# Performance work log

Hardware: AMD Instinct MI355X
Metric: run time of the kernel (lower is better)

## Reference

```python
import jax, jax.numpy as jnp
import numpy as np

CH = 512
GROUPS = 32
EPS = 1e-6


def setup_inputs() -> dict:
    key = jax.random.key(0)
    ks = jax.random.split(key, 12)
    b, c, h, w = 4, CH, 64, 64
    std = 1.0 / np.sqrt(c)
    return {
        "x": jax.random.normal(ks[0], (b, c, h, w), dtype=jnp.float32),
        "norm_gamma": jnp.ones((c,), jnp.float32),
        "norm_beta": jnp.zeros((c,), jnp.float32),
        "wq": jax.random.normal(ks[1], (c, c), jnp.float32) * std,
        "bq": jax.random.normal(ks[2], (c,), jnp.float32) * 0.01,
        "wk": jax.random.normal(ks[3], (c, c), jnp.float32) * std,
        "bk": jax.random.normal(ks[4], (c,), jnp.float32) * 0.01,
        "wv": jax.random.normal(ks[5], (c, c), jnp.float32) * std,
        "bv": jax.random.normal(ks[6], (c,), jnp.float32) * 0.01,
        "wo": jax.random.normal(ks[7], (c, c), jnp.float32) * std,
        "bo": jax.random.normal(ks[8], (c,), jnp.float32) * 0.01,
    }


def _group_norm(x, gamma, beta):
    b, c, h, w = x.shape
    xg = x.reshape(b, GROUPS, c // GROUPS, h, w)
    mean = xg.mean(axis=(2, 3, 4), keepdims=True)
    var = xg.var(axis=(2, 3, 4), keepdims=True)
    xn = ((xg - mean) * jax.lax.rsqrt(var + EPS)).reshape(b, c, h, w)
    return xn * gamma[None, :, None, None] + beta[None, :, None, None]


def reference(x, norm_gamma, norm_beta, wq, bq, wk, bk, wv, bv, wo, bo):
    b, c, h, w = x.shape
    hn = _group_norm(x, norm_gamma, norm_beta)
    hs = hn.reshape(b, c, h * w)  # [b, c, n]
    # 1x1 convs == per-pixel matmuls over channel dim (weight[out,in])
    q = jnp.einsum('oc,bcn->bno', wq, hs) + bq  # [b, n, c]
    k = jnp.einsum('oc,bcn->bon', wk, hs) + bk[None, :, None]  # [b, c, n]
    v = jnp.einsum('oc,bcn->bno', wv, hs) + bv  # [b, n, c]
    scale = c ** (-0.5)
    attn = jax.nn.softmax(jnp.einsum('bnc,bcm->bnm', q, k) * scale, axis=-1)
    out = jnp.einsum('bnm,bmc->bnc', attn, v)  # [b, n, c]
    out = jnp.einsum('oc,bnc->bon', wo, out) + bo[None, :, None]  # [b, c, n]
    return x + out.reshape(b, c, h, w)
```

## Files before the change

### kernel.cpp

```cpp
#include <hip/hip_runtime.h>
#include <hip/hip_bf16.h>
#include <cstdint>

typedef __bf16 bf16;
typedef __bf16 bf16x8 __attribute__((ext_vector_type(8)));
typedef __bf16 bf16x4 __attribute__((ext_vector_type(4)));
typedef float f32x4 __attribute__((ext_vector_type(4)));

__device__ __forceinline__ void gld_lds16(const void* g, void* l) {
  __builtin_amdgcn_global_load_lds((const __attribute__((address_space(1))) void*)g,
                                   (__attribute__((address_space(3))) void*)l, 16, 0, 0);
}

enum { BIAS_NONE = 0, BIAS_COL = 1, BIAS_ROW = 2, BIAS_QK = 3 };
enum { OUT_BF16 = 0, OUT_F32_RESID = 1, OUT_EXP = 2 };

template<int BIAS_MODE, int OUT_MODE>
__global__ __launch_bounds__(256)
void gemm_bt(const bf16* __restrict__ A, long sA, int lda,
             const bf16* __restrict__ Bm, long sB, int ldb,
             void* __restrict__ Cv, long sC, int ldc,
             const float* __restrict__ bias, const float* __restrict__ bias2,
             const float* __restrict__ resid, long sR,
             int K, float scale)
{
  const int bm = blockIdx.x, bn = blockIdx.y, bz = blockIdx.z;
  const char* Ab = (const char*)(A + (long)bz * sA);
  const char* Bb = (const char*)(Bm + (long)bz * sB);
  const int tid = threadIdx.x;
  const int wave = tid >> 6, lane = tid & 63;
  const int wr = wave >> 1, wc = wave & 1;

  __shared__ __attribute__((aligned(128))) char lds[32768];
  char* ldsA = lds;
  char* ldsB = lds + 16384;

  uint32_t aoff[4], boff[4];
#pragma unroll
  for (int i = 0; i < 4; ++i) {
    uint32_t ra = (uint32_t)(wr * 64 + i * 16 + (lane & 15));
    uint32_t la = ra * 128u + (uint32_t)((lane >> 4) << 4);
    aoff[i] = la ^ ((la >> 3) & 0x70u);
    uint32_t rb = (uint32_t)(wc * 64 + i * 16 + (lane & 15));
    uint32_t lb = rb * 128u + (uint32_t)((lane >> 4) << 4);
    boff[i] = lb ^ ((lb >> 3) & 0x70u);
  }
  uint32_t srow[4], sinb[4];
#pragma unroll
  for (int t = 0; t < 4; ++t) {
    uint32_t paddr = (uint32_t)(((wave * 4 + t) * 64 + lane) * 16);
    uint32_t laddr = paddr ^ ((paddr >> 3) & 0x70u);
    srow[t] = laddr >> 7;
    sinb[t] = laddr & 127u;
  }

  const long ldab = (long)lda * 2, ldbb = (long)ldb * 2;
  const long arow0 = (long)bm * 128, brow0 = (long)bn * 128;
  f32x4 acc[4][4] = {};
  const int nK = K >> 6;
  for (int kt = 0; kt < nK; ++kt) {
    const long k0b = (long)kt * 128;
#pragma unroll
    for (int t = 0; t < 4; ++t) {
      gld_lds16(Ab + (arow0 + srow[t]) * ldab + k0b + sinb[t], ldsA + (wave * 4 + t) * 1024);
      gld_lds16(Bb + (brow0 + srow[t]) * ldbb + k0b + sinb[t], ldsB + (wave * 4 + t) * 1024);
    }
    __syncthreads();
#pragma unroll
    for (int kk = 0; kk < 2; ++kk) {
      bf16x8 af[4], bfr[4];
#pragma unroll
      for (int i = 0; i < 4; ++i) {
        af[i]  = *(const bf16x8*)(ldsA + (aoff[i] ^ (kk << 6)));
        bfr[i] = *(const bf16x8*)(ldsB + (boff[i] ^ (kk << 6)));
      }
#pragma unroll
      for (int mi = 0; mi < 4; ++mi)
#pragma unroll
        for (int ni = 0; ni < 4; ++ni)
          acc[mi][ni] = __builtin_amdgcn_mfma_f32_16x16x32_bf16(af[mi], bfr[ni], acc[mi][ni], 0, 0, 0);
    }
    __syncthreads();
  }

  const int cl = lane & 15, rq = lane >> 4;
  const long row0 = (long)bm * 128 + wr * 64;
  const long col0 = (long)bn * 128 + wc * 64;

  if constexpr (OUT_MODE == OUT_F32_RESID) {
    float* Co = (float*)Cv + (long)bz * sC;
    const float* X = resid + (long)bz * sR;
#pragma unroll
    for (int mi = 0; mi < 4; ++mi)
#pragma unroll
      for (int ni = 0; ni < 4; ++ni) {
        const long col = col0 + ni * 16 + cl;
#pragma unroll
        for (int j = 0; j < 4; ++j) {
          const long row = row0 + mi * 16 + rq * 4 + j;
          Co[row * ldc + col] = acc[mi][ni][j] + bias[row] + X[row * ldc + col];
        }
      }
  } else if constexpr (BIAS_MODE == BIAS_QK) {
    const bool isq = (col0 < 512);
    bf16* base = (bf16*)Cv + (long)bz * sC + (isq ? 0 : sR);
    const long csub = isq ? 0 : 512;
#pragma unroll
    for (int mi = 0; mi < 4; ++mi)
#pragma unroll
      for (int ni = 0; ni < 4; ++ni) {
        const long col = col0 + ni * 16 + cl;
        const float bc = isq ? bias[col] * scale : bias2[col - 512];
        const float vs = isq ? scale : 1.f;
#pragma unroll
        for (int j = 0; j < 4; ++j) {
          const long row = row0 + mi * 16 + rq * 4 + j;
          base[row * ldc + (col - csub)] = (bf16)(acc[mi][ni][j] * vs + bc);
        }
      }
  } else {
    bf16* Co = (bf16*)Cv + (long)bz * sC;
#pragma unroll
    for (int mi = 0; mi < 4; ++mi)
#pragma unroll
      for (int ni = 0; ni < 4; ++ni) {
        const long col = col0 + ni * 16 + cl;
        float bc = 0.f;
        if (BIAS_MODE == BIAS_COL) bc = bias[col] * scale;
#pragma unroll
        for (int j = 0; j < 4; ++j) {
          const long row = row0 + mi * 16 + rq * 4 + j;
          float v = acc[mi][ni][j] * (BIAS_MODE == BIAS_COL ? scale : 1.f) + bc;
          if (BIAS_MODE == BIAS_ROW) v += bias[row];
          if constexpr (OUT_MODE == OUT_EXP) v = __expf(v);
          Co[row * ldc + col] = (bf16)v;
        }
      }
  }
}

__global__ __launch_bounds__(256, 2)
void gemm_pv7(const bf16* __restrict__ P, long sA,
              const bf16* __restrict__ Vm, long sB,
              bf16* __restrict__ O, long sC, int swz)
{
  constexpr int T = 64;
  extern __shared__ char lds[];
  char* ldsA = lds;
  char* ldsB = lds + 16384;

  int bm, bn, bz;
  if (swz) {
    const int bid = blockIdx.x;
    const int xcd = bid & 7;
    bz = xcd >> 1;
    bn = (bid >> 3) & 1;
    bm = ((bid >> 4) << 1) | (xcd & 1);
  } else { bm = blockIdx.x; bn = blockIdx.y; bz = blockIdx.z; }

  const char* Ab = (const char*)(P + (long)bz * sA) + (long)bm * 64 * 8192;
  const char* Bb = (const char*)(Vm + (long)bz * sB) + (long)bn * 256 * 8192;
  const int tid = threadIdx.x, wave = tid >> 6, lane = tid & 63;
  const int lg = lane >> 4, l15 = lane & 15;

  const uint32_t ar0 = (uint32_t)(tid >> 3), ac16 = (uint32_t)((tid & 7) * 16);
  const uint32_t aswz = (ar0 & 7) << 4;

  const uint32_t bdst0 = (uint32_t)tid * 16;

  uint32_t aO[4], bO[4];
#pragma unroll
  for (int mi = 0; mi < 4; ++mi) {
    uint32_t r = (uint32_t)(mi * 16 + l15);
    aO[mi] = r * 128 + (((uint32_t)(lg * 16)) ^ ((r & 7) << 4));
  }
#pragma unroll
  for (int ni = 0; ni < 4; ++ni) {
    uint32_t r = (uint32_t)(wave * 64 + ni * 16 + l15);
    bO[ni] = r * 128 + (((uint32_t)(lg * 16)) ^ ((r & 7) << 4));
  }

  f32x4 acc[4][4] = {};
  float lsum0 = 0.f, lsum1 = 0.f;

  auto stageB = [&](uint32_t nb, int t) {
#pragma unroll
    for (int j = 0; j < 8; ++j) {
      uint32_t row = (uint32_t)(j * 32) + ar0;
      gld_lds16(Bb + (long)row * 8192 + (long)t * 128 + (ac16 ^ ((row & 7) << 4)),
                ldsB + nb * 32768 + (uint32_t)(j * 4096) + bdst0);
    }
  };
  auto loadA0 = [&](int t) -> bf16x8 {
    return *(const bf16x8*)(Ab + (long)ar0 * 8192 + (long)t * 128 + ac16);
  };
  auto loadA1 = [&](int t) -> bf16x8 {
    return *(const bf16x8*)(Ab + (long)(32 + ar0) * 8192 + (long)t * 128 + ac16);
  };
  auto writeA = [&](uint32_t nb, bf16x8 p0, bf16x8 p1) {
#pragma unroll
    for (int j = 0; j < 8; ++j) {
      lsum0 += (float)p0[j];
      lsum1 += (float)p1[j];
    }
    *(bf16x8*)(ldsA + nb * 8192 + ar0 * 128 + (ac16 ^ aswz)) = p0;
    *(bf16x8*)(ldsA + nb * 8192 + (32 + ar0) * 128 + (ac16 ^ aswz)) = p1;
  };

  bf16x8 an0 = loadA0(0), an1 = loadA1(0);
  stageB(0, 0);
  writeA(0, an0, an1);
  an0 = loadA0(1); an1 = loadA1(1);
  asm volatile("s_waitcnt vmcnt(2)" ::: "memory");
  asm volatile("s_waitcnt lgkmcnt(0)" ::: "memory");
  __builtin_amdgcn_sched_barrier(0);
  __builtin_amdgcn_s_barrier();

  for (int t = 0; t < T; ++t) {
    const uint32_t cur = (uint32_t)(t & 1), nxt = cur ^ 1u;

    if (t + 1 < T) stageB(nxt, t + 1);
    if (t + 1 < T) writeA(nxt, an0, an1);
    if (t + 2 < T) { an0 = loadA0(t + 2); an1 = loadA1(t + 2); }

    bf16x8 af[4][2], bfr[4][2];
#pragma unroll
    for (int mi = 0; mi < 4; ++mi)
#pragma unroll
      for (int kk = 0; kk < 2; ++kk)
        af[mi][kk] = *(const bf16x8*)(ldsA + ((cur * 8192 + aO[mi]) ^ (uint32_t)(kk << 6)));
#pragma unroll
    for (int ni = 0; ni < 4; ++ni)
#pragma unroll
      for (int kk = 0; kk < 2; ++kk)
        bfr[ni][kk] = *(const bf16x8*)(ldsB + ((cur * 32768 + bO[ni]) ^ (uint32_t)(kk << 6)));

    __builtin_amdgcn_s_setprio(1);
#pragma unroll
    for (int mi = 0; mi < 4; ++mi)
#pragma unroll
      for (int ni = 0; ni < 4; ++ni)
#pragma unroll
        for (int kk = 0; kk < 2; ++kk)
          acc[mi][ni] = __builtin_amdgcn_mfma_f32_16x16x32_bf16(af[mi][kk], bfr[ni][kk], acc[mi][ni], 0, 0, 0);
    __builtin_amdgcn_s_setprio(0);

    if (t + 1 < T) {
      if (t + 2 < T) asm volatile("s_waitcnt vmcnt(2)" ::: "memory");
      else           asm volatile("s_waitcnt vmcnt(0)" ::: "memory");
      asm volatile("s_waitcnt lgkmcnt(0)" ::: "memory");
      __builtin_amdgcn_sched_barrier(0);
      __builtin_amdgcn_s_barrier();
    }
  }

  lsum0 += __shfl_xor(lsum0, 1, 64);
  lsum0 += __shfl_xor(lsum0, 2, 64);
  lsum0 += __shfl_xor(lsum0, 4, 64);
  lsum1 += __shfl_xor(lsum1, 1, 64);
  lsum1 += __shfl_xor(lsum1, 2, 64);
  lsum1 += __shfl_xor(lsum1, 4, 64);
  float* Lrow = (float*)ldsA;
  if ((tid & 7) == 0) {
    Lrow[ar0] = lsum0;
    Lrow[32 + ar0] = lsum1;
  }
  __syncthreads();

  bf16* Co = O + (long)bz * sC + (long)bm * 64 * 512 + (long)bn * 256;
#pragma unroll
  for (int mi = 0; mi < 4; ++mi)
#pragma unroll
    for (int j = 0; j < 4; ++j) {
      const int row = mi * 16 + lg * 4 + j;
      const float invL = 1.f / Lrow[row];
#pragma unroll
      for (int ni = 0; ni < 4; ++ni) {
        const int col = wave * 64 + ni * 16 + l15;
        Co[(long)row * 512 + col] = (bf16)(acc[mi][ni][j] * invL);
      }
    }
}

__global__ __launch_bounds__(256)
void gn_stats(const float* __restrict__ x, float* __restrict__ stats)
{
  const int bg = blockIdx.x;
  const float4* px = (const float4*)(x + (long)bg * 65536);
  float s1 = 0.f, s2 = 0.f;
  for (int i = threadIdx.x; i < 16384; i += 256) {
    float4 f = px[i];
    s1 += f.x + f.y + f.z + f.w;
    s2 += f.x * f.x + f.y * f.y + f.z * f.z + f.w * f.w;
  }
#pragma unroll
  for (int d = 32; d > 0; d >>= 1) {
    s1 += __shfl_xor(s1, d, 64);
    s2 += __shfl_xor(s2, d, 64);
  }
  __shared__ float r1[4], r2[4];
  const int wave = threadIdx.x >> 6, lane = threadIdx.x & 63;
  if (lane == 0) { r1[wave] = s1; r2[wave] = s2; }
  __syncthreads();
  if (threadIdx.x == 0) {
    float t1 = r1[0] + r1[1] + r1[2] + r1[3];
    float t2 = r2[0] + r2[1] + r2[2] + r2[3];
    float mean = t1 * (1.f / 65536.f);
    float var  = t2 * (1.f / 65536.f) - mean * mean;
    stats[bg * 2]     = mean;
    stats[bg * 2 + 1] = rsqrtf(var + 1e-6f);
  }
}

__global__ __launch_bounds__(256)
void gn_apply(const float* __restrict__ x, const float* __restrict__ stats,
              const float* __restrict__ gamma, const float* __restrict__ beta,
              bf16* __restrict__ hn)
{
  const int b = blockIdx.y;
  const int n0 = blockIdx.x * 64;
  __shared__ __attribute__((aligned(16))) char lt[65536];
  const int tid = threadIdx.x;
  for (int i = 0; i < 32; ++i) {
    int f = i * 256 + tid;
    int c = f >> 4;
    int n4 = f & 15;
    float4 xv = *(const float4*)(x + (((long)b * 512 + c) * 4096) + n0 + n4 * 4);
    int g = c >> 4;
    float mean = stats[(b * 32 + g) * 2];
    float rstd = stats[(b * 32 + g) * 2 + 1];
    float ga = gamma[c], be = beta[c];
    float y[4];
    y[0] = (xv.x - mean) * rstd * ga + be;
    y[1] = (xv.y - mean) * rstd * ga + be;
    y[2] = (xv.z - mean) * rstd * ga + be;
    y[3] = (xv.w - mean) * rstd * ga + be;
    uint32_t cb = (uint32_t)(c * 2);
#pragma unroll
    for (int jj = 0; jj < 4; ++jj) {
      uint32_t nl = (uint32_t)(n4 * 4 + jj);
      uint32_t phys = nl * 1024u + (cb ^ (((nl >> 2) & 7u) << 4));
      *(bf16*)(lt + phys) = (bf16)y[jj];
    }
  }
  __syncthreads();
  for (int i = 0; i < 16; ++i) {
    int j = i * 256 + tid;
    uint32_t row = (uint32_t)(j >> 6);
    uint32_t m = (uint32_t)(j & 63);
    uint32_t phys = row * 1024u + ((m * 16u) ^ (((row >> 2) & 7u) << 4));
    uint4 val = *(const uint4*)(lt + phys);
    *(uint4*)((char*)(hn + ((long)b * 4096 + n0 + row) * 512) + m * 16) = val;
  }
}

__global__ __launch_bounds__(256)
void conv_w4(const float* __restrict__ w0, const float* __restrict__ w1,
             const float* __restrict__ w2, const float* __restrict__ w3,
             bf16* __restrict__ dst)
{
  const int z = blockIdx.y;
  const float* src = (z == 0) ? w0 : (z == 1) ? w1 : (z == 2) ? w2 : w3;
  const int i = blockIdx.x * 256 + threadIdx.x;
  float4 f = ((const float4*)src)[i];
  bf16x4 o;
  o[0] = (bf16)f.x; o[1] = (bf16)f.y; o[2] = (bf16)f.z; o[3] = (bf16)f.w;
  ((bf16x4*)(dst))[(long)z * 65536 + i] = o;
}

extern "C" void kernel_launch(void* const* d_in, const int* in_sizes, int n_in,
                              void* d_out, int out_size, void* d_ws, size_t ws_size,
                              hipStream_t stream)
{
  const float* x     = (const float*)d_in[0];
  const float* gamma = (const float*)d_in[1];
  const float* beta  = (const float*)d_in[2];
  const float* wq = (const float*)d_in[3];
  const float* bq = (const float*)d_in[4];
  const float* wk = (const float*)d_in[5];
  const float* bk = (const float*)d_in[6];
  const float* wv = (const float*)d_in[7];
  const float* bv = (const float*)d_in[8];
  const float* wo = (const float*)d_in[9];
  const float* bo = (const float*)d_in[10];
  float* out = (float*)d_out;

  char* ws = (char*)d_ws;
  bf16* hn  = (bf16*)(ws + 0);
  bf16* q   = (bf16*)(ws + 16777216);
  bf16* k   = (bf16*)(ws + 33554432);
  bf16* v   = (bf16*)(ws + 50331648);
  bf16* O   = (bf16*)(ws + 67108864);
  bf16* wqb = (bf16*)(ws + 83886080);
  bf16* wvb = (bf16*)(ws + 84934656);
  bf16* wob = (bf16*)(ws + 85458944);
  float* gstats = (float*)(ws + 85983232);
  bf16* S   = (bf16*)(ws + 85984256);

  const long sBC = 2097152;
  const long sS1 = 16777216;
  const long K_OFS = 8388608;
  const float scale = 0.044194173824159216f;

  const int LDS_PV = 81920;
  hipFuncSetAttribute(reinterpret_cast<const void*>(gemm_pv7),
                      hipFuncAttributeMaxDynamicSharedMemorySize, LDS_PV);

  conv_w4<<<dim3(256, 4), 256, 0, stream>>>(wq, wk, wv, wo, wqb);
  gn_stats<<<128, 256, 0, stream>>>(x, gstats);
  gn_apply<<<dim3(64, 4), 256, 0, stream>>>(x, gstats, gamma, beta, hn);

  gemm_bt<BIAS_QK, OUT_BF16><<<dim3(32, 8, 4), 256, 0, stream>>>(
      hn, sBC, 512, wqb, 0, 512, q, sBC, 512,
      bq, bk, nullptr, K_OFS, 512, scale);
  gemm_bt<BIAS_ROW, OUT_BF16><<<dim3(4, 32, 4), 256, 0, stream>>>(
      wvb, 0, 512, hn, sBC, 512, v, sBC, 4096,
      bv, nullptr, nullptr, 0, 512, 1.f);

  const bool tier1 = ws_size >= (size_t)220202112;
  if (tier1) {
    gemm_bt<BIAS_NONE, OUT_EXP><<<dim3(32, 32, 4), 256, 0, stream>>>(
        q, sBC, 512, k, sBC, 512, S, sS1, 4096,
        nullptr, nullptr, nullptr, 0, 512, 1.f);
    gemm_pv7<<<dim3(512, 1, 1), 256, LDS_PV, stream>>>(
        S, sS1, v, sBC, O, sBC, 1);
  } else {
    for (int b = 0; b < 4; ++b) {
      gemm_bt<BIAS_NONE, OUT_EXP><<<dim3(32, 32, 1), 256, 0, stream>>>(
          q + b * sBC, 0, 512, k + b * sBC, 0, 512, S, 0, 4096,
          nullptr, nullptr, nullptr, 0, 512, 1.f);
      gemm_pv7<<<dim3(64, 2, 1), 256, LDS_PV, stream>>>(
          S, 0, v + b * sBC, 0, O + b * sBC, 0, 0);
    }
  }

  gemm_bt<BIAS_ROW, OUT_F32_RESID><<<dim3(4, 32, 4), 256, 0, stream>>>(
      wob, 0, 512, O, sBC, 512, out, sBC, 4096,
      bo, nullptr, x, sBC, 512, 1.f);
}
```

Measured before the change: 269.2 us.

## Halve PV K-tile to raise occupancy and swizzle QK^T blocks across XCDs

The PV kernel now uses a 32-wide K step (128 iterations instead of 64), with a new LDS layout, a new swizzle and half the LDS footprint. This allows launch bounds of 4 blocks per CU instead of 2, to improve latency hiding. The QK^T exp GEMM now runs on a flattened 1D grid that is remapped so neighbouring M-tiles land on the same XCD, to improve L2 reuse of the K operand. The trade-off is twice as many barriers per PV tile and lower register headroom per thread.

```diff
diff --git a/kernel.cpp b/kernel.cpp
--- a/kernel.cpp
+++ b/kernel.cpp
@@ -22,9 +22,17 @@
              void* __restrict__ Cv, long sC, int ldc,
              const float* __restrict__ bias, const float* __restrict__ bias2,
              const float* __restrict__ resid, long sR,
-             int K, float scale)
-{
-  const int bm = blockIdx.x, bn = blockIdx.y, bz = blockIdx.z;
+             int K, float scale, int swz)
+{
+  int bm, bn, bz;
+  if (swz) {
+    const int bid = blockIdx.x;
+    const int xcd = bid & 7;
+    const int i = bid >> 3;
+    bm = xcd * 4 + (i & 3);
+    bn = (i >> 2) & 31;
+    bz = i >> 7;
+  } else { bm = blockIdx.x; bn = blockIdx.y; bz = blockIdx.z; }
   const char* Ab = (const char*)(A + (long)bz * sA);
   const char* Bb = (const char*)(Bm + (long)bz * sB);
   const int tid = threadIdx.x;
@@ -37,13 +45,13 @@
 
   uint32_t aoff[4], boff[4];
 #pragma unroll
-  for (int i = 0; i < 4; ++i) {
-    uint32_t ra = (uint32_t)(wr * 64 + i * 16 + (lane & 15));
+  for (int i2 = 0; i2 < 4; ++i2) {
+    uint32_t ra = (uint32_t)(wr * 64 + i2 * 16 + (lane & 15));
     uint32_t la = ra * 128u + (uint32_t)((lane >> 4) << 4);
-    aoff[i] = la ^ ((la >> 3) & 0x70u);
-    uint32_t rb = (uint32_t)(wc * 64 + i * 16 + (lane & 15));
+    aoff[i2] = la ^ ((la >> 3) & 0x70u);
+    uint32_t rb = (uint32_t)(wc * 64 + i2 * 16 + (lane & 15));
     uint32_t lb = rb * 128u + (uint32_t)((lane >> 4) << 4);
-    boff[i] = lb ^ ((lb >> 3) & 0x70u);
+    boff[i2] = lb ^ ((lb >> 3) & 0x70u);
   }
   uint32_t srow[4], sinb[4];
 #pragma unroll
@@ -70,9 +78,9 @@
     for (int kk = 0; kk < 2; ++kk) {
       bf16x8 af[4], bfr[4];
 #pragma unroll
-      for (int i = 0; i < 4; ++i) {
-        af[i]  = *(const bf16x8*)(ldsA + (aoff[i] ^ (kk << 6)));
-        bfr[i] = *(const bf16x8*)(ldsB + (boff[i] ^ (kk << 6)));
+      for (int i2 = 0; i2 < 4; ++i2) {
+        af[i2]  = *(const bf16x8*)(ldsA + (aoff[i2] ^ (kk << 6)));
+        bfr[i2] = *(const bf16x8*)(ldsB + (boff[i2] ^ (kk << 6)));
       }
 #pragma unroll
       for (int mi = 0; mi < 4; ++mi)
@@ -139,15 +147,15 @@
   }
 }
 
-__global__ __launch_bounds__(256, 2)
-void gemm_pv7(const bf16* __restrict__ P, long sA,
+__global__ __launch_bounds__(256, 4)
+void gemm_pv8(const bf16* __restrict__ P, long sA,
               const bf16* __restrict__ Vm, long sB,
               bf16* __restrict__ O, long sC, int swz)
 {
-  constexpr int T = 64;
+  constexpr int T = 128;
   extern __shared__ char lds[];
   char* ldsA = lds;
-  char* ldsB = lds + 16384;
+  char* ldsB = lds + 8192;
 
   int bm, bn, bz;
   if (swz) {
@@ -163,55 +171,46 @@
   const int tid = threadIdx.x, wave = tid >> 6, lane = tid & 63;
   const int lg = lane >> 4, l15 = lane & 15;
 
-  const uint32_t ar0 = (uint32_t)(tid >> 3), ac16 = (uint32_t)((tid & 7) * 16);
-  const uint32_t aswz = (ar0 & 7) << 4;
-
-  const uint32_t bdst0 = (uint32_t)tid * 16;
+  const uint32_t ar = (uint32_t)(tid >> 2), ach = (uint32_t)((tid & 3) * 16);
+  const uint32_t aswz = ((ar >> 1) & 3u) << 4;
 
   uint32_t aO[4], bO[4];
 #pragma unroll
   for (int mi = 0; mi < 4; ++mi) {
     uint32_t r = (uint32_t)(mi * 16 + l15);
-    aO[mi] = r * 128 + (((uint32_t)(lg * 16)) ^ ((r & 7) << 4));
+    aO[mi] = r * 64 + (((uint32_t)(lg * 16)) ^ (((r >> 1) & 3u) << 4));
   }
 #pragma unroll
   for (int ni = 0; ni < 4; ++ni) {
     uint32_t r = (uint32_t)(wave * 64 + ni * 16 + l15);
-    bO[ni] = r * 128 + (((uint32_t)(lg * 16)) ^ ((r & 7) << 4));
+    bO[ni] = r * 64 + (((uint32_t)(lg * 16)) ^ (((r >> 1) & 3u) << 4));
   }
 
   f32x4 acc[4][4] = {};
-  float lsum0 = 0.f, lsum1 = 0.f;
+  float lsum = 0.f;
 
   auto stageB = [&](uint32_t nb, int t) {
 #pragma unroll
-    for (int j = 0; j < 8; ++j) {
-      uint32_t row = (uint32_t)(j * 32) + ar0;
-      gld_lds16(Bb + (long)row * 8192 + (long)t * 128 + (ac16 ^ ((row & 7) << 4)),
-                ldsB + nb * 32768 + (uint32_t)(j * 4096) + bdst0);
+    for (int j = 0; j < 4; ++j) {
+      uint32_t row = (uint32_t)(j * 64) + ar;
+      gld_lds16(Bb + (long)row * 8192 + (long)t * 64 + (ach ^ (((row >> 1) & 3u) << 4)),
+                ldsB + nb * 16384 + (uint32_t)(j * 4096) + (uint32_t)tid * 16);
     }
   };
-  auto loadA0 = [&](int t) -> bf16x8 {
-    return *(const bf16x8*)(Ab + (long)ar0 * 8192 + (long)t * 128 + ac16);
+  auto loadA = [&](int t) -> bf16x8 {
+    return *(const bf16x8*)(Ab + (long)ar * 8192 + (long)t * 64 + ach);
   };
-  auto loadA1 = [&](int t) -> bf16x8 {
-    return *(const bf16x8*)(Ab + (long)(32 + ar0) * 8192 + (long)t * 128 + ac16);
+  auto writeA = [&](uint32_t nb, bf16x8 p) {
+#pragma unroll
+    for (int j = 0; j < 8; ++j) lsum += (float)p[j];
+    *(bf16x8*)(ldsA + nb * 4096 + ar * 64 + (ach ^ aswz)) = p;
   };
-  auto writeA = [&](uint32_t nb, bf16x8 p0, bf16x8 p1) {
-#pragma unroll
-    for (int j = 0; j < 8; ++j) {
-      lsum0 += (float)p0[j];
-      lsum1 += (float)p1[j];
-    }
-    *(bf16x8*)(ldsA + nb * 8192 + ar0 * 128 + (ac16 ^ aswz)) = p0;
-    *(bf16x8*)(ldsA + nb * 8192 + (32 + ar0) * 128 + (ac16 ^ aswz)) = p1;
-  };
-
-  bf16x8 an0 = loadA0(0), an1 = loadA1(0);
+
+  bf16x8 an = loadA(0);
   stageB(0, 0);
-  writeA(0, an0, an1);
-  an0 = loadA0(1); an1 = loadA1(1);
-  asm volatile("s_waitcnt vmcnt(2)" ::: "memory");
+  writeA(0, an);
+  an = loadA(1);
+  asm volatile("s_waitcnt vmcnt(1)" ::: "memory");
   asm volatile("s_waitcnt lgkmcnt(0)" ::: "memory");
   __builtin_amdgcn_sched_barrier(0);
   __builtin_amdgcn_s_barrier();
@@ -220,33 +219,27 @@
     const uint32_t cur = (uint32_t)(t & 1), nxt = cur ^ 1u;
 
     if (t + 1 < T) stageB(nxt, t + 1);
-    if (t + 1 < T) writeA(nxt, an0, an1);
-    if (t + 2 < T) { an0 = loadA0(t + 2); an1 = loadA1(t + 2); }
-
-    bf16x8 af[4][2], bfr[4][2];
+    if (t + 1 < T) writeA(nxt, an);
+    if (t + 2 < T) an = loadA(t + 2);
+
+    bf16x8 af[4], bfr[4];
 #pragma unroll
     for (int mi = 0; mi < 4; ++mi)
-#pragma unroll
-      for (int kk = 0; kk < 2; ++kk)
-        af[mi][kk] = *(const bf16x8*)(ldsA + ((cur * 8192 + aO[mi]) ^ (uint32_t)(kk << 6)));
+      af[mi] = *(const bf16x8*)(ldsA + cur * 4096 + aO[mi]);
 #pragma unroll
     for (int ni = 0; ni < 4; ++ni)
-#pragma unroll
-      for (int kk = 0; kk < 2; ++kk)
-        bfr[ni][kk] = *(const bf16x8*)(ldsB + ((cur * 32768 + bO[ni]) ^ (uint32_t)(kk << 6)));
+      bfr[ni] = *(const bf16x8*)(ldsB + cur * 16384 + bO[ni]);
 
     __builtin_amdgcn_s_setprio(1);
 #pragma unroll
     for (int mi = 0; mi < 4; ++mi)
 #pragma unroll
       for (int ni = 0; ni < 4; ++ni)
-#pragma unroll
-        for (int kk = 0; kk < 2; ++kk)
-          acc[mi][ni] = __builtin_amdgcn_mfma_f32_16x16x32_bf16(af[mi][kk], bfr[ni][kk], acc[mi][ni], 0, 0, 0);
+        acc[mi][ni] = __builtin_amdgcn_mfma_f32_16x16x32_bf16(af[mi], bfr[ni], acc[mi][ni], 0, 0, 0);
     __builtin_amdgcn_s_setprio(0);
 
     if (t + 1 < T) {
-      if (t + 2 < T) asm volatile("s_waitcnt vmcnt(2)" ::: "memory");
+      if (t + 2 < T) asm volatile("s_waitcnt vmcnt(1)" ::: "memory");
       else           asm volatile("s_waitcnt vmcnt(0)" ::: "memory");
       asm volatile("s_waitcnt lgkmcnt(0)" ::: "memory");
       __builtin_amdgcn_sched_barrier(0);
@@ -254,17 +247,10 @@
     }
   }
 
-  lsum0 += __shfl_xor(lsum0, 1, 64);
-  lsum0 += __shfl_xor(lsum0, 2, 64);
-  lsum0 += __shfl_xor(lsum0, 4, 64);
-  lsum1 += __shfl_xor(lsum1, 1, 64);
-  lsum1 += __shfl_xor(lsum1, 2, 64);
-  lsum1 += __shfl_xor(lsum1, 4, 64);
+  lsum += __shfl_xor(lsum, 1, 64);
+  lsum += __shfl_xor(lsum, 2, 64);
   float* Lrow = (float*)ldsA;
-  if ((tid & 7) == 0) {
-    Lrow[ar0] = lsum0;
-    Lrow[32 + ar0] = lsum1;
-  }
+  if ((tid & 3) == 0) Lrow[ar] = lsum;
   __syncthreads();
 
   bf16* Co = O + (long)bz * sC + (long)bm * 64 * 512 + (long)bn * 256;
@@ -402,8 +388,8 @@
   const long K_OFS = 8388608;
   const float scale = 0.044194173824159216f;
 
-  const int LDS_PV = 81920;
-  hipFuncSetAttribute(reinterpret_cast<const void*>(gemm_pv7),
+  const int LDS_PV = 40960;
+  hipFuncSetAttribute(reinterpret_cast<const void*>(gemm_pv8),
                       hipFuncAttributeMaxDynamicSharedMemorySize, LDS_PV);
 
   conv_w4<<<dim3(256, 4), 256, 0, stream>>>(wq, wk, wv, wo, wqb);
@@ -412,29 +398,29 @@
 
   gemm_bt<BIAS_QK, OUT_BF16><<<dim3(32, 8, 4), 256, 0, stream>>>(
       hn, sBC, 512, wqb, 0, 512, q, sBC, 512,
-      bq, bk, nullptr, K_OFS, 512, scale);
+      bq, bk, nullptr, K_OFS, 512, scale, 0);
   gemm_bt<BIAS_ROW, OUT_BF16><<<dim3(4, 32, 4), 256, 0, stream>>>(
       wvb, 0, 512, hn, sBC, 512, v, sBC, 4096,
-      bv, nullptr, nullptr, 0, 512, 1.f);
+      bv, nullptr, nullptr, 0, 512, 1.f, 0);
 
   const bool tier1 = ws_size >= (size_t)220202112;
   if (tier1) {
-    gemm_bt<BIAS_NONE, OUT_EXP><<<dim3(32, 32, 4), 256, 0, stream>>>(
+    gemm_bt<BIAS_NONE, OUT_EXP><<<dim3(4096, 1, 1), 256, 0, stream>>>(
         q, sBC, 512, k, sBC, 512, S, sS1, 4096,
-        nullptr, nullptr, nullptr, 0, 512, 1.f);
-    gemm_pv7<<<dim3(512, 1, 1), 256, LDS_PV, stream>>>(
+        nullptr, nullptr, nullptr, 0, 512, 1.f, 1);
+    gemm_pv8<<<dim3(512, 1, 1), 256, LDS_PV, stream>>>(
         S, sS1, v, sBC, O, sBC, 1);
   } else {
     for (int b = 0; b < 4; ++b) {
       gemm_bt<BIAS_NONE, OUT_EXP><<<dim3(32, 32, 1), 256, 0, stream>>>(
           q + b * sBC, 0, 512, k + b * sBC, 0, 512, S, 0, 4096,
-          nullptr, nullptr, nullptr, 0, 512, 1.f);
-      gemm_pv7<<<dim3(64, 2, 1), 256, LDS_PV, stream>>>(
+          nullptr, nullptr, nullptr, 0, 512, 1.f, 0);
+      gemm_pv8<<<dim3(64, 2, 1), 256, LDS_PV, stream>>>(
           S, 0, v + b * sBC, 0, O + b * sBC, 0, 0);
     }
   }
 
   gemm_bt<BIAS_ROW, OUT_F32_RESID><<<dim3(4, 32, 4), 256, 0, stream>>>(
       wob, 0, 512, O, sBC, 512, out, sBC, 4096,
-      bo, nullptr, x, sBC, 512, 1.f);
-}
+      bo, nullptr, x, sBC, 512, 1.f, 0);
+}
```

Result: slower. 299.4 us (+11.2%).

## Load P fragments directly into registers and compute row sums via MFMA with ones

Applied to the files above, without the earlier changes.

The PV GEMM kernel stops staging the P (exp-scores) tile through LDS. Each wave now loads its A fragments straight from global memory into double-buffered registers. The softmax row sums are computed with an extra MFMA against a ones vector instead of scalar adds, shuffles and an LDS reduction. This cuts LDS traffic and usage (64KB instead of 80KB) and removes the final sync, at the cost of every wave redundantly loading the same P rows from global or cache and using more registers.

```diff
diff --git a/kernel.cpp b/kernel.cpp
--- a/kernel.cpp
+++ b/kernel.cpp
@@ -140,14 +140,13 @@
 }
 
 __global__ __launch_bounds__(256, 2)
-void gemm_pv7(const bf16* __restrict__ P, long sA,
-              const bf16* __restrict__ Vm, long sB,
-              bf16* __restrict__ O, long sC, int swz)
+void gemm_pv10(const bf16* __restrict__ P, long sA,
+               const bf16* __restrict__ Vm, long sB,
+               bf16* __restrict__ O, long sC, int swz)
 {
   constexpr int T = 64;
   extern __shared__ char lds[];
-  char* ldsA = lds;
-  char* ldsB = lds + 16384;
+  char* ldsB = lds;
 
   int bm, bn, bz;
   if (swz) {
@@ -164,16 +163,14 @@
   const int lg = lane >> 4, l15 = lane & 15;
 
   const uint32_t ar0 = (uint32_t)(tid >> 3), ac16 = (uint32_t)((tid & 7) * 16);
-  const uint32_t aswz = (ar0 & 7) << 4;
-
   const uint32_t bdst0 = (uint32_t)tid * 16;
 
-  uint32_t aO[4], bO[4];
-#pragma unroll
-  for (int mi = 0; mi < 4; ++mi) {
-    uint32_t r = (uint32_t)(mi * 16 + l15);
-    aO[mi] = r * 128 + (((uint32_t)(lg * 16)) ^ ((r & 7) << 4));
-  }
+  const char* aBase[4];
+#pragma unroll
+  for (int mi = 0; mi < 4; ++mi)
+    aBase[mi] = Ab + (long)(mi * 16 + l15) * 8192 + lg * 16;
+
+  uint32_t bO[4];
 #pragma unroll
   for (int ni = 0; ni < 4; ++ni) {
     uint32_t r = (uint32_t)(wave * 64 + ni * 16 + l15);
@@ -181,7 +178,10 @@
   }
 
   f32x4 acc[4][4] = {};
-  float lsum0 = 0.f, lsum1 = 0.f;
+  f32x4 acc_l[4] = {};
+  bf16x8 ones;
+#pragma unroll
+  for (int j = 0; j < 8; ++j) ones[j] = (bf16)1.0f;
 
   auto stageB = [&](uint32_t nb, int t) {
 #pragma unroll
@@ -191,44 +191,27 @@
                 ldsB + nb * 32768 + (uint32_t)(j * 4096) + bdst0);
     }
   };
-  auto loadA0 = [&](int t) -> bf16x8 {
-    return *(const bf16x8*)(Ab + (long)ar0 * 8192 + (long)t * 128 + ac16);
+  auto loadA = [&](bf16x8 (&a)[4][2], int t) {
+#pragma unroll
+    for (int mi = 0; mi < 4; ++mi)
+#pragma unroll
+      for (int kk = 0; kk < 2; ++kk)
+        a[mi][kk] = *(const bf16x8*)(aBase[mi] + (long)t * 128 + kk * 64);
   };
-  auto loadA1 = [&](int t) -> bf16x8 {
-    return *(const bf16x8*)(Ab + (long)(32 + ar0) * 8192 + (long)t * 128 + ac16);
-  };
-  auto writeA = [&](uint32_t nb, bf16x8 p0, bf16x8 p1) {
-#pragma unroll
-    for (int j = 0; j < 8; ++j) {
-      lsum0 += (float)p0[j];
-      lsum1 += (float)p1[j];
-    }
-    *(bf16x8*)(ldsA + nb * 8192 + ar0 * 128 + (ac16 ^ aswz)) = p0;
-    *(bf16x8*)(ldsA + nb * 8192 + (32 + ar0) * 128 + (ac16 ^ aswz)) = p1;
-  };
-
-  bf16x8 an0 = loadA0(0), an1 = loadA1(0);
+
+  bf16x8 aE[4][2], aO_[4][2];
+
   stageB(0, 0);
-  writeA(0, an0, an1);
-  an0 = loadA0(1); an1 = loadA1(1);
-  asm volatile("s_waitcnt vmcnt(2)" ::: "memory");
-  asm volatile("s_waitcnt lgkmcnt(0)" ::: "memory");
+  loadA(aE, 0);
+  asm volatile("s_waitcnt vmcnt(8)" ::: "memory");
   __builtin_amdgcn_sched_barrier(0);
   __builtin_amdgcn_s_barrier();
 
-  for (int t = 0; t < T; ++t) {
+  auto body = [&](int t, bf16x8 (&aUse)[4][2], bf16x8 (&aNxt)[4][2]) {
     const uint32_t cur = (uint32_t)(t & 1), nxt = cur ^ 1u;
-
-    if (t + 1 < T) stageB(nxt, t + 1);
-    if (t + 1 < T) writeA(nxt, an0, an1);
-    if (t + 2 < T) { an0 = loadA0(t + 2); an1 = loadA1(t + 2); }
-
-    bf16x8 af[4][2], bfr[4][2];
-#pragma unroll
-    for (int mi = 0; mi < 4; ++mi)
-#pragma unroll
-      for (int kk = 0; kk < 2; ++kk)
-        af[mi][kk] = *(const bf16x8*)(ldsA + ((cur * 8192 + aO[mi]) ^ (uint32_t)(kk << 6)));
+    if (t + 1 < T) { stageB(nxt, t + 1); loadA(aNxt, t + 1); }
+
+    bf16x8 bfr[4][2];
 #pragma unroll
     for (int ni = 0; ni < 4; ++ni)
 #pragma unroll
@@ -237,35 +220,29 @@
 
     __builtin_amdgcn_s_setprio(1);
 #pragma unroll
-    for (int mi = 0; mi < 4; ++mi)
-#pragma unroll
-      for (int ni = 0; ni < 4; ++ni)
-#pragma unroll
-        for (int kk = 0; kk < 2; ++kk)
-          acc[mi][ni] = __builtin_amdgcn_mfma_f32_16x16x32_bf16(af[mi][kk], bfr[ni][kk], acc[mi][ni], 0, 0, 0);
+    for (int kk = 0; kk < 2; ++kk)
+#pragma unroll
+      for (int mi = 0; mi < 4; ++mi) {
+        acc_l[mi] = __builtin_amdgcn_mfma_f32_16x16x32_bf16(aUse[mi][kk], ones, acc_l[mi], 0, 0, 0);
+#pragma unroll
+        for (int ni = 0; ni < 4; ++ni)
+          acc[mi][ni] = __builtin_amdgcn_mfma_f32_16x16x32_bf16(aUse[mi][kk], bfr[ni][kk], acc[mi][ni], 0, 0, 0);
+      }
     __builtin_amdgcn_s_setprio(0);
 
     if (t + 1 < T) {
-      if (t + 2 < T) asm volatile("s_waitcnt vmcnt(2)" ::: "memory");
-      else           asm volatile("s_waitcnt vmcnt(0)" ::: "memory");
+      asm volatile("s_waitcnt vmcnt(8)" ::: "memory");
       asm volatile("s_waitcnt lgkmcnt(0)" ::: "memory");
       __builtin_amdgcn_sched_barrier(0);
       __builtin_amdgcn_s_barrier();
     }
-  }
-
-  lsum0 += __shfl_xor(lsum0, 1, 64);
-  lsum0 += __shfl_xor(lsum0, 2, 64);
-  lsum0 += __shfl_xor(lsum0, 4, 64);
-  lsum1 += __shfl_xor(lsum1, 1, 64);
-  lsum1 += __shfl_xor(lsum1, 2, 64);
-  lsum1 += __shfl_xor(lsum1, 4, 64);
-  float* Lrow = (float*)ldsA;
-  if ((tid & 7) == 0) {
-    Lrow[ar0] = lsum0;
-    Lrow[32 + ar0] = lsum1;
-  }
-  __syncthreads();
+  };
+
+#pragma unroll 1
+  for (int t2 = 0; t2 < T; t2 += 2) {
+    body(t2, aE, aO_);
+    body(t2 + 1, aO_, aE);
+  }
 
   bf16* Co = O + (long)bz * sC + (long)bm * 64 * 512 + (long)bn * 256;
 #pragma unroll
@@ -273,7 +250,7 @@
 #pragma unroll
     for (int j = 0; j < 4; ++j) {
       const int row = mi * 16 + lg * 4 + j;
-      const float invL = 1.f / Lrow[row];
+      const float invL = 1.f / acc_l[mi][j];
 #pragma unroll
       for (int ni = 0; ni < 4; ++ni) {
         const int col = wave * 64 + ni * 16 + l15;
@@ -402,8 +379,8 @@
   const long K_OFS = 8388608;
   const float scale = 0.044194173824159216f;
 
-  const int LDS_PV = 81920;
-  hipFuncSetAttribute(reinterpret_cast<const void*>(gemm_pv7),
+  const int LDS_PV = 65536;
+  hipFuncSetAttribute(reinterpret_cast<const void*>(gemm_pv10),
                       hipFuncAttributeMaxDynamicSharedMemorySize, LDS_PV);
 
   conv_w4<<<dim3(256, 4), 256, 0, stream>>>(wq, wk, wv, wo, wqb);
@@ -422,14 +399,14 @@
     gemm_bt<BIAS_NONE, OUT_EXP><<<dim3(32, 32, 4), 256, 0, stream>>>(
         q, sBC, 512, k, sBC, 512, S, sS1, 4096,
         nullptr, nullptr, nullptr, 0, 512, 1.f);
-    gemm_pv7<<<dim3(512, 1, 1), 256, LDS_PV, stream>>>(
+    gemm_pv10<<<dim3(512, 1, 1), 256, LDS_PV, stream>>>(
         S, sS1, v, sBC, O, sBC, 1);
   } else {
     for (int b = 0; b < 4; ++b) {
       gemm_bt<BIAS_NONE, OUT_EXP><<<dim3(32, 32, 1), 256, 0, stream>>>(
           q + b * sBC, 0, 512, k + b * sBC, 0, 512, S, 0, 4096,
           nullptr, nullptr, nullptr, 0, 512, 1.f);
-      gemm_pv7<<<dim3(64, 2, 1), 256, LDS_PV, stream>>>(
+      gemm_pv10<<<dim3(64, 2, 1), 256, LDS_PV, stream>>>(
           S, 0, v + b * sBC, 0, O + b * sBC, 0, 0);
     }
   }
```

Measured after the change: 343.6 us. +27.6%, slower.

## Store V pre-tiled and load PV B-operand directly from global into registers

Applied to the files above, without the earlier changes.

The V projection now writes V in a k-blocked tiled layout (8 contiguous channels per 16-byte chunk), so the PV kernel can fetch B fragments straight from global memory into registers instead of staging them through LDS. This cuts LDS from 80KB to 16KB per block, removing the B LDS writes and reads and the associated waits, with registers double-buffered across an unrolled pair of iterations. The cost is that each wave reads B directly from global/L2 with no intra-block sharing, and the V epilogue now does scattered stores.

```diff
diff --git a/kernel.cpp b/kernel.cpp
--- a/kernel.cpp
+++ b/kernel.cpp
@@ -13,7 +13,7 @@
 }
 
 enum { BIAS_NONE = 0, BIAS_COL = 1, BIAS_ROW = 2, BIAS_QK = 3 };
-enum { OUT_BF16 = 0, OUT_F32_RESID = 1, OUT_EXP = 2 };
+enum { OUT_BF16 = 0, OUT_F32_RESID = 1, OUT_EXP = 2, OUT_VTILED = 3 };
 
 template<int BIAS_MODE, int OUT_MODE>
 __global__ __launch_bounds__(256)
@@ -101,6 +101,20 @@
           Co[row * ldc + col] = acc[mi][ni][j] + bias[row] + X[row * ldc + col];
         }
       }
+  } else if constexpr (OUT_MODE == OUT_VTILED) {
+    bf16* Vt = (bf16*)Cv + (long)bz * sC;
+#pragma unroll
+    for (int mi = 0; mi < 4; ++mi)
+#pragma unroll
+      for (int ni = 0; ni < 4; ++ni) {
+        const long col = col0 + ni * 16 + cl;
+#pragma unroll
+        for (int j = 0; j < 4; ++j) {
+          const long row = row0 + mi * 16 + rq * 4 + j;
+          float v = acc[mi][ni][j] + bias[row];
+          Vt[((col >> 3) * 512 + row) * 8 + (col & 7)] = (bf16)v;
+        }
+      }
   } else if constexpr (BIAS_MODE == BIAS_QK) {
     const bool isq = (col0 < 512);
     bf16* base = (bf16*)Cv + (long)bz * sC + (isq ? 0 : sR);
@@ -140,14 +154,13 @@
 }
 
 __global__ __launch_bounds__(256, 2)
-void gemm_pv7(const bf16* __restrict__ P, long sA,
-              const bf16* __restrict__ Vm, long sB,
-              bf16* __restrict__ O, long sC, int swz)
+void gemm_pv11(const bf16* __restrict__ P, long sA,
+               const bf16* __restrict__ Vt, long sVt,
+               bf16* __restrict__ O, long sC, int swz)
 {
   constexpr int T = 64;
   extern __shared__ char lds[];
   char* ldsA = lds;
-  char* ldsB = lds + 16384;
 
   int bm, bn, bz;
   if (swz) {
@@ -159,37 +172,35 @@
   } else { bm = blockIdx.x; bn = blockIdx.y; bz = blockIdx.z; }
 
   const char* Ab = (const char*)(P + (long)bz * sA) + (long)bm * 64 * 8192;
-  const char* Bb = (const char*)(Vm + (long)bz * sB) + (long)bn * 256 * 8192;
+  const char* Btb = (const char*)(Vt + (long)bz * sVt);
   const int tid = threadIdx.x, wave = tid >> 6, lane = tid & 63;
   const int lg = lane >> 4, l15 = lane & 15;
 
   const uint32_t ar0 = (uint32_t)(tid >> 3), ac16 = (uint32_t)((tid & 7) * 16);
   const uint32_t aswz = (ar0 & 7) << 4;
 
-  const uint32_t bdst0 = (uint32_t)tid * 16;
-
-  uint32_t aO[4], bO[4];
+  uint32_t aO[4];
 #pragma unroll
   for (int mi = 0; mi < 4; ++mi) {
     uint32_t r = (uint32_t)(mi * 16 + l15);
     aO[mi] = r * 128 + (((uint32_t)(lg * 16)) ^ ((r & 7) << 4));
   }
+  uint32_t colb[4];
 #pragma unroll
   for (int ni = 0; ni < 4; ++ni) {
-    uint32_t r = (uint32_t)(wave * 64 + ni * 16 + l15);
-    bO[ni] = r * 128 + (((uint32_t)(lg * 16)) ^ ((r & 7) << 4));
+    uint32_t col = (uint32_t)(bn * 256 + wave * 64 + ni * 16 + l15);
+    colb[ni] = col * 16 + (uint32_t)lg * 8192;
   }
 
   f32x4 acc[4][4] = {};
   float lsum0 = 0.f, lsum1 = 0.f;
 
-  auto stageB = [&](uint32_t nb, int t) {
-#pragma unroll
-    for (int j = 0; j < 8; ++j) {
-      uint32_t row = (uint32_t)(j * 32) + ar0;
-      gld_lds16(Bb + (long)row * 8192 + (long)t * 128 + (ac16 ^ ((row & 7) << 4)),
-                ldsB + nb * 32768 + (uint32_t)(j * 4096) + bdst0);
-    }
+  auto loadB = [&](bf16x8 (&b)[4][2], int t) {
+#pragma unroll
+    for (int ni = 0; ni < 4; ++ni)
+#pragma unroll
+      for (int kk = 0; kk < 2; ++kk)
+        b[ni][kk] = *(const bf16x8*)(Btb + (long)t * 65536 + kk * 32768 + colb[ni]);
   };
   auto loadA0 = [&](int t) -> bf16x8 {
     return *(const bf16x8*)(Ab + (long)ar0 * 8192 + (long)t * 128 + ac16);
@@ -207,34 +218,30 @@
     *(bf16x8*)(ldsA + nb * 8192 + (32 + ar0) * 128 + (ac16 ^ aswz)) = p1;
   };
 
-  bf16x8 an0 = loadA0(0), an1 = loadA1(0);
-  stageB(0, 0);
+  bf16x8 bE[4][2], bO_[4][2];
+  bf16x8 an0, an1;
+
+  loadB(bE, 0);
+  an0 = loadA0(0); an1 = loadA1(0);
   writeA(0, an0, an1);
   an0 = loadA0(1); an1 = loadA1(1);
-  asm volatile("s_waitcnt vmcnt(2)" ::: "memory");
   asm volatile("s_waitcnt lgkmcnt(0)" ::: "memory");
   __builtin_amdgcn_sched_barrier(0);
   __builtin_amdgcn_s_barrier();
 
-  for (int t = 0; t < T; ++t) {
+  auto body = [&](int t, bf16x8 (&bCur)[4][2], bf16x8 (&bNxt)[4][2]) {
     const uint32_t cur = (uint32_t)(t & 1), nxt = cur ^ 1u;
 
-    if (t + 1 < T) stageB(nxt, t + 1);
+    if (t + 1 < T) loadB(bNxt, t + 1);
+    bf16x8 af[4][2];
+#pragma unroll
+    for (int mi = 0; mi < 4; ++mi)
+#pragma unroll
+      for (int kk = 0; kk < 2; ++kk)
+        af[mi][kk] = *(const bf16x8*)(ldsA + ((cur * 8192 + aO[mi]) ^ (uint32_t)(kk << 6)));
     if (t + 1 < T) writeA(nxt, an0, an1);
     if (t + 2 < T) { an0 = loadA0(t + 2); an1 = loadA1(t + 2); }
 
-    bf16x8 af[4][2], bfr[4][2];
-#pragma unroll
-    for (int mi = 0; mi < 4; ++mi)
-#pragma unroll
-      for (int kk = 0; kk < 2; ++kk)
-        af[mi][kk] = *(const bf16x8*)(ldsA + ((cur * 8192 + aO[mi]) ^ (uint32_t)(kk << 6)));
-#pragma unroll
-    for (int ni = 0; ni < 4; ++ni)
-#pragma unroll
-      for (int kk = 0; kk < 2; ++kk)
-        bfr[ni][kk] = *(const bf16x8*)(ldsB + ((cur * 32768 + bO[ni]) ^ (uint32_t)(kk << 6)));
-
     __builtin_amdgcn_s_setprio(1);
 #pragma unroll
     for (int mi = 0; mi < 4; ++mi)
@@ -242,16 +249,20 @@
       for (int ni = 0; ni < 4; ++ni)
 #pragma unroll
         for (int kk = 0; kk < 2; ++kk)
-          acc[mi][ni] = __builtin_amdgcn_mfma_f32_16x16x32_bf16(af[mi][kk], bfr[ni][kk], acc[mi][ni], 0, 0, 0);
+          acc[mi][ni] = __builtin_amdgcn_mfma_f32_16x16x32_bf16(af[mi][kk], bCur[ni][kk], acc[mi][ni], 0, 0, 0);
     __builtin_amdgcn_s_setprio(0);
 
     if (t + 1 < T) {
-      if (t + 2 < T) asm volatile("s_waitcnt vmcnt(2)" ::: "memory");
-      else           asm volatile("s_waitcnt vmcnt(0)" ::: "memory");
       asm volatile("s_waitcnt lgkmcnt(0)" ::: "memory");
       __builtin_amdgcn_sched_barrier(0);
       __builtin_amdgcn_s_barrier();
     }
+  };
+
+#pragma unroll 1
+  for (int t2 = 0; t2 < T; t2 += 2) {
+    body(t2, bE, bO_);
+    body(t2 + 1, bO_, bE);
   }
 
   lsum0 += __shfl_xor(lsum0, 1, 64);
@@ -402,8 +413,8 @@
   const long K_OFS = 8388608;
   const float scale = 0.044194173824159216f;
 
-  const int LDS_PV = 81920;
-  hipFuncSetAttribute(reinterpret_cast<const void*>(gemm_pv7),
+  const int LDS_PV = 16384;
+  hipFuncSetAttribute(reinterpret_cast<const void*>(gemm_pv11),
                       hipFuncAttributeMaxDynamicSharedMemorySize, LDS_PV);
 
   conv_w4<<<dim3(256, 4), 256, 0, stream>>>(wq, wk, wv, wo, wqb);
@@ -413,7 +424,7 @@
   gemm_bt<BIAS_QK, OUT_BF16><<<dim3(32, 8, 4), 256, 0, stream>>>(
       hn, sBC, 512, wqb, 0, 512, q, sBC, 512,
       bq, bk, nullptr, K_OFS, 512, scale);
-  gemm_bt<BIAS_ROW, OUT_BF16><<<dim3(4, 32, 4), 256, 0, stream>>>(
+  gemm_bt<BIAS_ROW, OUT_VTILED><<<dim3(4, 32, 4), 256, 0, stream>>>(
       wvb, 0, 512, hn, sBC, 512, v, sBC, 4096,
       bv, nullptr, nullptr, 0, 512, 1.f);
 
@@ -422,14 +433,14 @@
     gemm_bt<BIAS_NONE, OUT_EXP><<<dim3(32, 32, 4), 256, 0, stream>>>(
         q, sBC, 512, k, sBC, 512, S, sS1, 4096,
         nullptr, nullptr, nullptr, 0, 512, 1.f);
-    gemm_pv7<<<dim3(512, 1, 1), 256, LDS_PV, stream>>>(
+    gemm_pv11<<<dim3(512, 1, 1), 256, LDS_PV, stream>>>(
         S, sS1, v, sBC, O, sBC, 1);
   } else {
     for (int b = 0; b < 4; ++b) {
       gemm_bt<BIAS_NONE, OUT_EXP><<<dim3(32, 32, 1), 256, 0, stream>>>(
           q + b * sBC, 0, 512, k + b * sBC, 0, 512, S, 0, 4096,
           nullptr, nullptr, nullptr, 0, 512, 1.f);
-      gemm_pv7<<<dim3(64, 2, 1), 256, LDS_PV, stream>>>(
+      gemm_pv11<<<dim3(64, 2, 1), 256, LDS_PV, stream>>>(
           S, 0, v + b * sBC, 0, O + b * sBC, 0, 0);
     }
   }
```

After: 264.5 us (median of 3 runs). Within noise of the previous version (-1.8%).
